# Performance work log

Measured on AMD Instinct MI355X. Metric: run time of the kernel, lower is better.

## Reference

```python
import jax, jax.numpy as jnp
import numpy as np

N_NODES = 50000
N_EDGES = 800000
IN_DIM = 256
HID = 32
HEADS = 8
OUT_DIM = 16
NEG_SLOPE = 0.2


def setup_inputs() -> dict:
    key = jax.random.key(0)
    ks = jax.random.split(key, 12)
    s = 0.05
    return {
        "emb": jax.random.normal(ks[0], (N_NODES, IN_DIM), jnp.float32),
        "src": jax.random.randint(ks[1], (N_EDGES,), 0, N_NODES),
        "dst": jax.random.randint(ks[2], (N_EDGES,), 0, N_NODES),
        "W1": jax.random.normal(ks[3], (IN_DIM, HEADS * HID), jnp.float32) * s,
        "attn_l1": jax.random.normal(ks[4], (HEADS, HID), jnp.float32) * s,
        "attn_r1": jax.random.normal(ks[5], (HEADS, HID), jnp.float32) * s,
        "bias1": jax.random.normal(ks[6], (HEADS * HID,), jnp.float32) * s,
        "W2": jax.random.normal(ks[7], (HEADS * HID, OUT_DIM), jnp.float32) * s,
        "attn_l2": jax.random.normal(ks[8], (1, OUT_DIM), jnp.float32) * s,
        "attn_r2": jax.random.normal(ks[9], (1, OUT_DIM), jnp.float32) * s,
        "bias2": jax.random.normal(ks[10], (OUT_DIM,), jnp.float32) * s,
    }


def gat_conv(x, src, dst, W, attn_l, attn_r, bias, n_heads, d_out):
    # x: [N, F_in] -> per-head projection h: [N, H, D]
    n = x.shape[0]
    h = (x @ W).reshape(n, n_heads, d_out)
    el = jnp.sum(h * attn_l, axis=-1)  # [N, H]
    er = jnp.sum(h * attn_r, axis=-1)  # [N, H]
    # edge scores with LeakyReLU (DGL negative_slope=0.2)
    e = jax.nn.leaky_relu(el[src] + er[dst], NEG_SLOPE)  # [E, H]
    # edge softmax over incoming edges of each destination node
    m = jax.ops.segment_max(e, dst, num_segments=n)  # [N, H]
    ee = jnp.exp(e - m[dst])
    denom = jax.ops.segment_sum(ee, dst, num_segments=n)  # [N, H]
    alpha = ee / denom[dst]  # [E, H]
    # weighted scatter-sum aggregation
    out = jax.ops.segment_sum(h[src] * alpha[:, :, None], dst, num_segments=n)  # [N, H, D]
    return out + bias.reshape(1, n_heads, d_out)


def reference(emb, src, dst, W1, attn_l1, attn_r1, bias1, W2, attn_l2, attn_r2, bias2):
    h = gat_conv(emb, src, dst, W1, attn_l1, attn_r1, bias1, HEADS, HID)  # [N, 8, 32]
    h = jax.nn.elu(h.reshape(N_NODES, HEADS * HID))  # [N, 256]
    out = gat_conv(h, src, dst, W2, attn_l2, attn_r2, bias2, 1, OUT_DIM)  # [N, 1, 16]
    return jnp.squeeze(out, axis=1)  # [N, 16]
```

## Files before the change

### kernel.cpp

```cpp
#include <hip/hip_runtime.h>
#include <math.h>

#define N_NODES 50000
#define N_EDGES 800000
#define NEG_SLOPE 0.2f

typedef __attribute__((ext_vector_type(8))) short bf16x8;
typedef __attribute__((ext_vector_type(4))) float f32x4;
typedef __attribute__((ext_vector_type(4))) _Float16 half4;

__device__ inline unsigned short f32_to_bf16_rn(float x) {
    unsigned u = __builtin_bit_cast(unsigned, x);
    unsigned r = u + 0x7fffu + ((u >> 16) & 1u);
    return (unsigned short)(r >> 16);
}
__device__ inline float bf16_bits_to_f32(unsigned short h) {
    unsigned u = ((unsigned)h) << 16;
    return __builtin_bit_cast(float, u);
}
__device__ inline void load_lds16(const void* g, void* l) {
    __builtin_amdgcn_global_load_lds(
        (const __attribute__((address_space(1))) void*)g,
        (__attribute__((address_space(3))) void*)l, 16, 0, 0);
}


__global__ void count_deg(const int* __restrict__ dst, int* __restrict__ deg) {
    int i = blockIdx.x * 256 + threadIdx.x;
    if (i < N_EDGES) atomicAdd(&deg[dst[i]], 1);
}

__global__ void scan_block(const int* __restrict__ deg, int* __restrict__ tmp,
                           int* __restrict__ bsum) {
    __shared__ int buf[256];
    int tid = threadIdx.x;
    int i = blockIdx.x * 256 + tid;
    int v = (i < N_NODES) ? deg[i] : 0;
    buf[tid] = v;
    __syncthreads();
    for (int off = 1; off < 256; off <<= 1) {
        int x = (tid >= off) ? buf[tid - off] : 0;
        __syncthreads();
        buf[tid] += x;
        __syncthreads();
    }
    if (i < N_NODES) tmp[i] = buf[tid];
    if (tid == 255) bsum[blockIdx.x] = buf[255];
}

__global__ void scan_bsum(int* __restrict__ bsum, int nb) {
    __shared__ int buf[256];
    int tid = threadIdx.x;
    int v = (tid < nb) ? bsum[tid] : 0;
    buf[tid] = v;
    __syncthreads();
    for (int off = 1; off < 256; off <<= 1) {
        int x = (tid >= off) ? buf[tid - off] : 0;
        __syncthreads();
        buf[tid] += x;
        __syncthreads();
    }
    if (tid < nb) bsum[tid] = buf[tid] - v;
}

__global__ void finalize_offs(const int* __restrict__ tmp, const int* __restrict__ deg,
                              const int* __restrict__ bsum, int* __restrict__ offs,
                              int* __restrict__ cursor) {
    int i = blockIdx.x * 256 + threadIdx.x;
    if (i < N_NODES) {
        int incl = tmp[i] + bsum[i >> 8];
        offs[i + 1] = incl;
        cursor[i] = incl - deg[i];
        if (i == 0) offs[0] = 0;
    }
}

__global__ void scatter_edges(const int* __restrict__ src, const int* __restrict__ dst,
                              int* __restrict__ cursor, int* __restrict__ src_csr) {
    int i = blockIdx.x * 256 + threadIdx.x;
    if (i < N_EDGES) {
        int p = atomicAdd(&cursor[dst[i]], 1);
        src_csr[p] = src[i];
    }
}


__global__ void convert_W1T(const float* __restrict__ W,
                            unsigned short* __restrict__ Th,
                            unsigned short* __restrict__ Tl) {
    int n = blockIdx.x;
    int k = threadIdx.x;
    float x = W[k * 256 + n];
    unsigned short h = f32_to_bf16_rn(x);
    float lo = x - bf16_bits_to_f32(h);
    size_t idx = ((size_t)(k >> 3) * 256 + n) * 8 + (k & 7);
    Th[idx] = h;
    Tl[idx] = f32_to_bf16_rn(lo);
}


__global__ __launch_bounds__(256) void gemm1_fused(const float* __restrict__ A,
                                                   const unsigned short* __restrict__ BTh,
                                                   const unsigned short* __restrict__ BTl,
                                                   const float* __restrict__ al,
                                                   const float* __restrict__ ar,
                                                   _Float16* __restrict__ C,
                                                   float* __restrict__ el,
                                                   float* __restrict__ er, int M) {
    __shared__ unsigned short Ah[4][64][8], Al[4][64][8];
    __shared__ unsigned short Bh[4][256][8], Bl[4][256][8];
    int tid = threadIdx.x;
    int lane = tid & 63, wave = tid >> 6;
    int kgl = lane >> 4, rl = lane & 15;
    int row0 = blockIdx.x * 64;

    f32x4 acc[4][4];
#pragma unroll
    for (int i = 0; i < 4; i++)
#pragma unroll
        for (int j = 0; j < 4; j++) acc[i][j] = (f32x4){0.f, 0.f, 0.f, 0.f};

    for (int k0 = 0; k0 < 256; k0 += 32) {
        int s0 = k0 >> 3;
#pragma unroll
        for (int i = 0; i < 4; i++) {
            load_lds16(&BTh[((size_t)(s0 + i) * 256 + tid) * 8], &Bh[i][wave << 6][0]);
            load_lds16(&BTl[((size_t)(s0 + i) * 256 + tid) * 8], &Bl[i][wave << 6][0]);
        }
        {
            int row = tid >> 2, kg = tid & 3;
            int gr = row0 + row;
            float4 x0 = make_float4(0.f, 0.f, 0.f, 0.f);
            float4 x1 = make_float4(0.f, 0.f, 0.f, 0.f);
            if (gr < M) {
                const float* p = &A[(size_t)gr * 256 + k0 + kg * 8];
                x0 = *reinterpret_cast<const float4*>(p);
                x1 = *reinterpret_cast<const float4*>(p + 4);
            }
            float xs[8] = {x0.x, x0.y, x0.z, x0.w, x1.x, x1.y, x1.z, x1.w};
            unsigned short hs[8], ls[8];
#pragma unroll
            for (int j = 0; j < 8; j++) {
                hs[j] = f32_to_bf16_rn(xs[j]);
                ls[j] = f32_to_bf16_rn(xs[j] - bf16_bits_to_f32(hs[j]));
            }
            *reinterpret_cast<bf16x8*>(&Ah[kg][row][0]) = *reinterpret_cast<bf16x8*>(hs);
            *reinterpret_cast<bf16x8*>(&Al[kg][row][0]) = *reinterpret_cast<bf16x8*>(ls);
        }
        __syncthreads();
        bf16x8 a_h[4], a_l[4];
#pragma unroll
        for (int mf = 0; mf < 4; mf++) {
            int row = mf * 16 + rl;
            a_h[mf] = *reinterpret_cast<bf16x8*>(&Ah[kgl][row][0]);
            a_l[mf] = *reinterpret_cast<bf16x8*>(&Al[kgl][row][0]);
        }
#pragma unroll
        for (int nf = 0; nf < 4; nf++) {
            int col = wave * 64 + nf * 16 + rl;
            bf16x8 bh = *reinterpret_cast<bf16x8*>(&Bh[kgl][col][0]);
            bf16x8 bl = *reinterpret_cast<bf16x8*>(&Bl[kgl][col][0]);
#pragma unroll
            for (int mf = 0; mf < 4; mf++) {
                acc[mf][nf] = __builtin_amdgcn_mfma_f32_16x16x32_bf16(a_h[mf], bh, acc[mf][nf], 0, 0, 0);
                acc[mf][nf] = __builtin_amdgcn_mfma_f32_16x16x32_bf16(a_h[mf], bl, acc[mf][nf], 0, 0, 0);
                acc[mf][nf] = __builtin_amdgcn_mfma_f32_16x16x32_bf16(a_l[mf], bh, acc[mf][nf], 0, 0, 0);
            }
        }
        __syncthreads();
    }
    float alv[4], arv[4];
#pragma unroll
    for (int nf = 0; nf < 4; nf++) {
        int c = wave * 64 + nf * 16 + rl;
        alv[nf] = al[c];
        arv[nf] = ar[c];
    }
#pragma unroll
    for (int mf = 0; mf < 4; mf++) {
#pragma unroll
        for (int rr = 0; rr < 4; rr++) {
            int grow = row0 + mf * 16 + (lane >> 4) * 4 + rr;
            bool ok = grow < M;
            if (ok) {
#pragma unroll
                for (int nf = 0; nf < 4; nf++) {
                    int gcol = wave * 64 + nf * 16 + rl;
                    C[(size_t)grow * 256 + gcol] = (_Float16)acc[mf][nf][rr];
                }
            }
            float e0 = acc[mf][0][rr] * alv[0] + acc[mf][1][rr] * alv[1];
            float e1 = acc[mf][2][rr] * alv[2] + acc[mf][3][rr] * alv[3];
            float f0 = acc[mf][0][rr] * arv[0] + acc[mf][1][rr] * arv[1];
            float f1 = acc[mf][2][rr] * arv[2] + acc[mf][3][rr] * arv[3];
#pragma unroll
            for (int off = 8; off >= 1; off >>= 1) {
                e0 += __shfl_down(e0, off, 16);
                e1 += __shfl_down(e1, off, 16);
                f0 += __shfl_down(f0, off, 16);
                f1 += __shfl_down(f1, off, 16);
            }
            if (rl == 0 && ok) {
                int h0 = wave * 2;
                el[grow * 8 + h0] = e0;
                el[grow * 8 + h0 + 1] = e1;
                er[grow * 8 + h0] = f0;
                er[grow * 8 + h0 + 1] = f1;
            }
        }
    }
}


__global__ __launch_bounds__(64) void agg1_fused(const int* __restrict__ offs,
                                                 const int* __restrict__ src_csr,
                                                 const float* __restrict__ el,
                                                 const float* __restrict__ er,
                                                 const _Float16* __restrict__ h1h,
                                                 const float* __restrict__ bias1,
                                                 _Float16* __restrict__ x2) {
    __shared__ float sc[64][8];
    int v = blockIdx.x;
    int t = threadIdx.x;
    int head = t >> 3, slot = t & 7;
    int start = offs[v], end = offs[v + 1];
    int deg = end - start;
    int ncache = (deg < 64) ? deg : 64;
    float erv = er[v * 8 + head];
    float s = 0.f;
    for (int base = 0; base < ncache; base += 8) {
        int e = base + slot;
        if (e < ncache) {
            int u = src_csr[start + e];
            float x = el[u * 8 + head] + erv;
            x = (x >= 0.f) ? x : NEG_SLOPE * x;
            float ex = expf(x);
            sc[e][head] = ex;
            s += ex;
        }
    }
    for (int base = 64; base < deg; base += 8) {
        int e = base + slot;
        if (e < deg) {
            int u = src_csr[start + e];
            float x = el[u * 8 + head] + erv;
            x = (x >= 0.f) ? x : NEG_SLOPE * x;
            s += expf(x);
        }
    }
    s += __shfl_xor(s, 1);
    s += __shfl_xor(s, 2);
    s += __shfl_xor(s, 4);
    float invs = (s > 0.f) ? 1.f / s : 0.f;
    __syncthreads();
    float4 acc = make_float4(0.f, 0.f, 0.f, 0.f);
    int i = start;
    for (; i + 3 < end && (i - start) + 3 < 64; i += 4) {
        int e = i - start;
        int u0 = src_csr[i];
        int u1 = src_csr[i + 1];
        int u2 = src_csr[i + 2];
        int u3 = src_csr[i + 3];
        float a0 = sc[e][head] * invs;
        float a1 = sc[e + 1][head] * invs;
        float a2 = sc[e + 2][head] * invs;
        float a3 = sc[e + 3][head] * invs;
        half4 p0 = *reinterpret_cast<const half4*>(&h1h[(size_t)u0 * 256 + 4 * t]);
        half4 p1 = *reinterpret_cast<const half4*>(&h1h[(size_t)u1 * 256 + 4 * t]);
        half4 p2 = *reinterpret_cast<const half4*>(&h1h[(size_t)u2 * 256 + 4 * t]);
        half4 p3 = *reinterpret_cast<const half4*>(&h1h[(size_t)u3 * 256 + 4 * t]);
        acc.x += a0 * (float)p0[0] + a1 * (float)p1[0] + a2 * (float)p2[0] + a3 * (float)p3[0];
        acc.y += a0 * (float)p0[1] + a1 * (float)p1[1] + a2 * (float)p2[1] + a3 * (float)p3[1];
        acc.z += a0 * (float)p0[2] + a1 * (float)p1[2] + a2 * (float)p2[2] + a3 * (float)p3[2];
        acc.w += a0 * (float)p0[3] + a1 * (float)p1[3] + a2 * (float)p2[3] + a3 * (float)p3[3];
    }
    for (; i < end; i++) {
        int e = i - start;
        int u0 = src_csr[i];
        float a0;
        if (e < 64) {
            a0 = sc[e][head] * invs;
        } else {
            float x = el[u0 * 8 + head] + erv;
            x = (x >= 0.f) ? x : NEG_SLOPE * x;
            a0 = expf(x) * invs;
        }
        half4 p0 = *reinterpret_cast<const half4*>(&h1h[(size_t)u0 * 256 + 4 * t]);
        acc.x += a0 * (float)p0[0];
        acc.y += a0 * (float)p0[1];
        acc.z += a0 * (float)p0[2];
        acc.w += a0 * (float)p0[3];
    }
    float4 b = *reinterpret_cast<const float4*>(&bias1[4 * t]);
    float ox = acc.x + b.x, oy = acc.y + b.y, oz = acc.z + b.z, ow = acc.w + b.w;
    ox = (ox > 0.f) ? ox : (expf(ox) - 1.f);
    oy = (oy > 0.f) ? oy : (expf(oy) - 1.f);
    oz = (oz > 0.f) ? oz : (expf(oz) - 1.f);
    ow = (ow > 0.f) ? ow : (expf(ow) - 1.f);
    half4 o = {(_Float16)ox, (_Float16)oy, (_Float16)oz, (_Float16)ow};
    *reinterpret_cast<half4*>(&x2[(size_t)v * 256 + 4 * t]) = o;
}


__global__ __launch_bounds__(256) void gemm2_mfma(const _Float16* __restrict__ X,
                                                  const float* __restrict__ W2,
                                                  const float* __restrict__ al,
                                                  const float* __restrict__ ar,
                                                  float* __restrict__ h2,
                                                  float* __restrict__ el2,
                                                  float* __restrict__ er2, int M) {
    __shared__ unsigned short Xh[4][64][8], Xl[4][64][8];
    __shared__ unsigned short Wh[32][16][8], Wl[32][16][8];
    int tid = threadIdx.x;
    int lane = tid & 63, wave = tid >> 6;
    int kgl = lane >> 4, rl = lane & 15;
    int row0 = blockIdx.x * 64;

#pragma unroll
    for (int j = 0; j < 16; j++) {
        int e = tid * 16 + j;
        float x = W2[e];
        unsigned short h = f32_to_bf16_rn(x);
        unsigned short l = f32_to_bf16_rn(x - bf16_bits_to_f32(h));
        int k = e >> 4, c = e & 15;
        Wh[k >> 3][c][k & 7] = h;
        Wl[k >> 3][c][k & 7] = l;
    }
    __syncthreads();

    f32x4 acc = (f32x4){0.f, 0.f, 0.f, 0.f};
    for (int k0 = 0; k0 < 256; k0 += 32) {
        {
            int row = tid >> 2, kg = tid & 3;
            int gr = row0 + row;
            unsigned short hs[8], ls[8];
            if (gr < M) {
                half4 x0 = *reinterpret_cast<const half4*>(&X[(size_t)gr * 256 + k0 + kg * 8]);
                half4 x1 = *reinterpret_cast<const half4*>(&X[(size_t)gr * 256 + k0 + kg * 8 + 4]);
                float xs[8] = {(float)x0[0], (float)x0[1], (float)x0[2], (float)x0[3],
                               (float)x1[0], (float)x1[1], (float)x1[2], (float)x1[3]};
#pragma unroll
                for (int j = 0; j < 8; j++) {
                    hs[j] = f32_to_bf16_rn(xs[j]);
                    ls[j] = f32_to_bf16_rn(xs[j] - bf16_bits_to_f32(hs[j]));
                }
            } else {
#pragma unroll
                for (int j = 0; j < 8; j++) { hs[j] = 0; ls[j] = 0; }
            }
            *reinterpret_cast<bf16x8*>(&Xh[kg][row][0]) = *reinterpret_cast<bf16x8*>(hs);
            *reinterpret_cast<bf16x8*>(&Xl[kg][row][0]) = *reinterpret_cast<bf16x8*>(ls);
        }
        __syncthreads();
        bf16x8 a_h = *reinterpret_cast<bf16x8*>(&Xh[kgl][wave * 16 + rl][0]);
        bf16x8 a_l = *reinterpret_cast<bf16x8*>(&Xl[kgl][wave * 16 + rl][0]);
        int kg = (k0 >> 3) + kgl;
        bf16x8 b_h = *reinterpret_cast<bf16x8*>(&Wh[kg][rl][0]);
        bf16x8 b_l = *reinterpret_cast<bf16x8*>(&Wl[kg][rl][0]);
        acc = __builtin_amdgcn_mfma_f32_16x16x32_bf16(a_h, b_h, acc, 0, 0, 0);
        acc = __builtin_amdgcn_mfma_f32_16x16x32_bf16(a_h, b_l, acc, 0, 0, 0);
        acc = __builtin_amdgcn_mfma_f32_16x16x32_bf16(a_l, b_h, acc, 0, 0, 0);
        __syncthreads();
    }
    float alv = al[rl], arv = ar[rl];
#pragma unroll
    for (int rr = 0; rr < 4; rr++) {
        int grow = row0 + wave * 16 + (lane >> 4) * 4 + rr;
        bool ok = grow < M;
        if (ok) h2[(size_t)grow * 16 + rl] = acc[rr];
        float pl = acc[rr] * alv;
        float pr = acc[rr] * arv;
#pragma unroll
        for (int off = 8; off >= 1; off >>= 1) {
            pl += __shfl_down(pl, off, 16);
            pr += __shfl_down(pr, off, 16);
        }
        if (rl == 0 && ok) {
            el2[grow] = pl;
            er2[grow] = pr;
        }
    }
}


__global__ __launch_bounds__(64) void agg2_fused(const int* __restrict__ offs,
                                                 const int* __restrict__ src_csr,
                                                 const float* __restrict__ el2,
                                                 const float* __restrict__ er2,
                                                 const float* __restrict__ h2,
                                                 const float* __restrict__ bias2,
                                                 float* __restrict__ out) {
    int v = blockIdx.x;
    int t = threadIdx.x;
    int start = offs[v], end = offs[v + 1];
    float erv = er2[v];
    float s = 0.f;
    for (int i = start + t; i < end; i += 64) {
        int u = src_csr[i];
        float x = el2[u] + erv;
        x = (x >= 0.f) ? x : NEG_SLOPE * x;
        s += expf(x);
    }
#pragma unroll
    for (int off = 32; off >= 1; off >>= 1) s += __shfl_xor(s, off);
    float invs = (s > 0.f) ? 1.f / s : 0.f;
    int eg = t >> 4, d = t & 15;
    float acc = 0.f;
    for (int i = start + eg; i < end; i += 4) {
        int u = src_csr[i];
        float x = el2[u] + erv;
        x = (x >= 0.f) ? x : NEG_SLOPE * x;
        acc += expf(x) * invs * h2[(size_t)u * 16 + d];
    }
    acc += __shfl_xor(acc, 32);
    acc += __shfl_xor(acc, 16);
    if (t < 16) out[(size_t)v * 16 + t] = acc + bias2[t];
}


extern "C" void kernel_launch(void* const* d_in, const int* in_sizes, int n_in,
                              void* d_out, int out_size, void* d_ws, size_t ws_size,
                              hipStream_t stream) {
    const float* emb   = (const float*)d_in[0];
    const int*   src   = (const int*)d_in[1];
    const int*   dst   = (const int*)d_in[2];
    const float* W1    = (const float*)d_in[3];
    const float* al1   = (const float*)d_in[4];
    const float* ar1   = (const float*)d_in[5];
    const float* bias1 = (const float*)d_in[6];
    const float* W2    = (const float*)d_in[7];
    const float* al2   = (const float*)d_in[8];
    const float* ar2   = (const float*)d_in[9];
    const float* bias2 = (const float*)d_in[10];
    float* out = (float*)d_out;

    char* ws = (char*)d_ws;
    auto alloc = [&](size_t bytes) -> void* {
        void* p = ws;
        ws += (bytes + 255) & ~(size_t)255;
        return p;
    };
    int* deg     = (int*)alloc(N_NODES * 4);
    int* cursor  = (int*)alloc(N_NODES * 4);
    int* offs    = (int*)alloc((N_NODES + 1) * 4);
    int* tmp     = (int*)alloc(N_NODES * 4);
    int* bsum    = (int*)alloc(256 * 4);
    int* src_csr = (int*)alloc(N_EDGES * 4);
    unsigned short* W1Th = (unsigned short*)alloc(256 * 256 * 2);
    unsigned short* W1Tl = (unsigned short*)alloc(256 * 256 * 2);
    _Float16* h1h = (_Float16*)alloc((size_t)N_NODES * 256 * 2);
    float* el1   = (float*)alloc(N_NODES * 8 * 4);
    float* er1   = (float*)alloc(N_NODES * 8 * 4);
    _Float16* x2h = (_Float16*)alloc((size_t)N_NODES * 256 * 2);
    float* h2    = (float*)alloc((size_t)N_NODES * 16 * 4);
    float* el2   = (float*)alloc(N_NODES * 4);
    float* er2   = (float*)alloc(N_NODES * 4);

    int nb = (N_NODES + 255) / 256;

    hipMemsetAsync(deg, 0, N_NODES * 4, stream);
    count_deg<<<(N_EDGES + 255) / 256, 256, 0, stream>>>(dst, deg);
    scan_block<<<nb, 256, 0, stream>>>(deg, tmp, bsum);
    scan_bsum<<<1, 256, 0, stream>>>(bsum, nb);
    finalize_offs<<<nb, 256, 0, stream>>>(tmp, deg, bsum, offs, cursor);
    scatter_edges<<<(N_EDGES + 255) / 256, 256, 0, stream>>>(src, dst, cursor, src_csr);

    convert_W1T<<<256, 256, 0, stream>>>(W1, W1Th, W1Tl);
    gemm1_fused<<<(N_NODES + 63) / 64, 256, 0, stream>>>(emb, W1Th, W1Tl, al1, ar1,
                                                         h1h, el1, er1, N_NODES);
    agg1_fused<<<N_NODES, 64, 0, stream>>>(offs, src_csr, el1, er1, h1h, bias1, x2h);
    gemm2_mfma<<<(N_NODES + 63) / 64, 256, 0, stream>>>(x2h, W2, al2, ar2, h2, el2, er2, N_NODES);
    agg2_fused<<<N_NODES, 64, 0, stream>>>(offs, src_csr, el2, er2, h2, bias2, out);
}
```

Measured before the change: 254.4 us.

## Fuse block-sum scan into finalize, prefetch GEMM1 A, widen GEMM2 K-steps, cache agg2 scores

Drops the separate scan_bsum launch by having each finalize block reduce the preceding block sums itself. GEMM1 now register-prefetches the next A tile while the current step computes, to hide global-load latency. GEMM2 stages 128 K-values per barrier instead of 32, cutting synchronisations from eight rounds to two at the cost of more LDS. agg2 caches up to 64 per-edge exp scores in shared memory so the second pass skips recomputing them.

```diff
diff --git a/kernel.cpp b/kernel.cpp
--- a/kernel.cpp
+++ b/kernel.cpp
@@ -48,27 +48,22 @@
     if (tid == 255) bsum[blockIdx.x] = buf[255];
 }
 
-__global__ void scan_bsum(int* __restrict__ bsum, int nb) {
-    __shared__ int buf[256];
-    int tid = threadIdx.x;
-    int v = (tid < nb) ? bsum[tid] : 0;
-    buf[tid] = v;
-    __syncthreads();
-    for (int off = 1; off < 256; off <<= 1) {
-        int x = (tid >= off) ? buf[tid - off] : 0;
-        __syncthreads();
-        buf[tid] += x;
-        __syncthreads();
-    }
-    if (tid < nb) bsum[tid] = buf[tid] - v;
-}
-
 __global__ void finalize_offs(const int* __restrict__ tmp, const int* __restrict__ deg,
                               const int* __restrict__ bsum, int* __restrict__ offs,
-                              int* __restrict__ cursor) {
-    int i = blockIdx.x * 256 + threadIdx.x;
+                              int* __restrict__ cursor, int nb) {
+    __shared__ int red[256];
+    int tid = threadIdx.x;
+    int b = blockIdx.x;
+    red[tid] = (tid < nb && tid < b) ? bsum[tid] : 0;
+    __syncthreads();
+    for (int off = 128; off > 0; off >>= 1) {
+        if (tid < off) red[tid] += red[tid + off];
+        __syncthreads();
+    }
+    int prefix = red[0];
+    int i = b * 256 + tid;
     if (i < N_NODES) {
-        int incl = tmp[i] + bsum[i >> 8];
+        int incl = tmp[i] + prefix;
         offs[i + 1] = incl;
         cursor[i] = incl - deg[i];
         if (i == 0) offs[0] = 0;
@@ -120,34 +115,40 @@
 #pragma unroll
         for (int j = 0; j < 4; j++) acc[i][j] = (f32x4){0.f, 0.f, 0.f, 0.f};
 
-    for (int k0 = 0; k0 < 256; k0 += 32) {
+    int rowA = tid >> 2, kgA = tid & 3;
+    int grA = row0 + rowA;
+    const float* pA = &A[(size_t)grA * 256 + kgA * 8];
+    float4 x0 = make_float4(0.f, 0.f, 0.f, 0.f);
+    float4 x1 = make_float4(0.f, 0.f, 0.f, 0.f);
+    if (grA < M) {
+        x0 = *reinterpret_cast<const float4*>(pA);
+        x1 = *reinterpret_cast<const float4*>(pA + 4);
+    }
+
+    for (int step = 0; step < 8; step++) {
+        int k0 = step * 32;
+        {
+            float xs[8] = {x0.x, x0.y, x0.z, x0.w, x1.x, x1.y, x1.z, x1.w};
+            unsigned short hs[8], ls[8];
+#pragma unroll
+            for (int j = 0; j < 8; j++) {
+                hs[j] = f32_to_bf16_rn(xs[j]);
+                ls[j] = f32_to_bf16_rn(xs[j] - bf16_bits_to_f32(hs[j]));
+            }
+            *reinterpret_cast<bf16x8*>(&Ah[kgA][rowA][0]) = *reinterpret_cast<bf16x8*>(hs);
+            *reinterpret_cast<bf16x8*>(&Al[kgA][rowA][0]) = *reinterpret_cast<bf16x8*>(ls);
+        }
         int s0 = k0 >> 3;
 #pragma unroll
         for (int i = 0; i < 4; i++) {
             load_lds16(&BTh[((size_t)(s0 + i) * 256 + tid) * 8], &Bh[i][wave << 6][0]);
             load_lds16(&BTl[((size_t)(s0 + i) * 256 + tid) * 8], &Bl[i][wave << 6][0]);
         }
-        {
-            int row = tid >> 2, kg = tid & 3;
-            int gr = row0 + row;
-            float4 x0 = make_float4(0.f, 0.f, 0.f, 0.f);
-            float4 x1 = make_float4(0.f, 0.f, 0.f, 0.f);
-            if (gr < M) {
-                const float* p = &A[(size_t)gr * 256 + k0 + kg * 8];
-                x0 = *reinterpret_cast<const float4*>(p);
-                x1 = *reinterpret_cast<const float4*>(p + 4);
-            }
-            float xs[8] = {x0.x, x0.y, x0.z, x0.w, x1.x, x1.y, x1.z, x1.w};
-            unsigned short hs[8], ls[8];
-#pragma unroll
-            for (int j = 0; j < 8; j++) {
-                hs[j] = f32_to_bf16_rn(xs[j]);
-                ls[j] = f32_to_bf16_rn(xs[j] - bf16_bits_to_f32(hs[j]));
-            }
-            *reinterpret_cast<bf16x8*>(&Ah[kg][row][0]) = *reinterpret_cast<bf16x8*>(hs);
-            *reinterpret_cast<bf16x8*>(&Al[kg][row][0]) = *reinterpret_cast<bf16x8*>(ls);
-        }
-        __syncthreads();
+        __syncthreads();
+        if (step < 7 && grA < M) {
+            x0 = *reinterpret_cast<const float4*>(pA + (step + 1) * 32);
+            x1 = *reinterpret_cast<const float4*>(pA + (step + 1) * 32 + 4);
+        }
         bf16x8 a_h[4], a_l[4];
 #pragma unroll
         for (int mf = 0; mf < 4; mf++) {
@@ -309,7 +310,7 @@
                                                   float* __restrict__ h2,
                                                   float* __restrict__ el2,
                                                   float* __restrict__ er2, int M) {
-    __shared__ unsigned short Xh[4][64][8], Xl[4][64][8];
+    __shared__ unsigned short Xh[16][64][8], Xl[16][64][8];
     __shared__ unsigned short Wh[32][16][8], Wl[32][16][8];
     int tid = threadIdx.x;
     int lane = tid & 63, wave = tid >> 6;
@@ -326,40 +327,46 @@
         Wh[k >> 3][c][k & 7] = h;
         Wl[k >> 3][c][k & 7] = l;
     }
-    __syncthreads();
 
     f32x4 acc = (f32x4){0.f, 0.f, 0.f, 0.f};
-    for (int k0 = 0; k0 < 256; k0 += 32) {
-        {
-            int row = tid >> 2, kg = tid & 3;
-            int gr = row0 + row;
+    int rowX = tid >> 2, kgb = (tid & 3) * 4;
+    int grX = row0 + rowX;
+    for (int step = 0; step < 2; step++) {
+#pragma unroll
+        for (int j = 0; j < 4; j++) {
+            int kg = kgb + j;
+            int kglob = step * 128 + kg * 8;
             unsigned short hs[8], ls[8];
-            if (gr < M) {
-                half4 x0 = *reinterpret_cast<const half4*>(&X[(size_t)gr * 256 + k0 + kg * 8]);
-                half4 x1 = *reinterpret_cast<const half4*>(&X[(size_t)gr * 256 + k0 + kg * 8 + 4]);
-                float xs[8] = {(float)x0[0], (float)x0[1], (float)x0[2], (float)x0[3],
-                               (float)x1[0], (float)x1[1], (float)x1[2], (float)x1[3]};
-#pragma unroll
-                for (int j = 0; j < 8; j++) {
-                    hs[j] = f32_to_bf16_rn(xs[j]);
-                    ls[j] = f32_to_bf16_rn(xs[j] - bf16_bits_to_f32(hs[j]));
+            if (grX < M) {
+                half4 a0 = *reinterpret_cast<const half4*>(&X[(size_t)grX * 256 + kglob]);
+                half4 a1 = *reinterpret_cast<const half4*>(&X[(size_t)grX * 256 + kglob + 4]);
+                float xs[8] = {(float)a0[0], (float)a0[1], (float)a0[2], (float)a0[3],
+                               (float)a1[0], (float)a1[1], (float)a1[2], (float)a1[3]};
+#pragma unroll
+                for (int q = 0; q < 8; q++) {
+                    hs[q] = f32_to_bf16_rn(xs[q]);
+                    ls[q] = f32_to_bf16_rn(xs[q] - bf16_bits_to_f32(hs[q]));
                 }
             } else {
 #pragma unroll
-                for (int j = 0; j < 8; j++) { hs[j] = 0; ls[j] = 0; }
-            }
-            *reinterpret_cast<bf16x8*>(&Xh[kg][row][0]) = *reinterpret_cast<bf16x8*>(hs);
-            *reinterpret_cast<bf16x8*>(&Xl[kg][row][0]) = *reinterpret_cast<bf16x8*>(ls);
-        }
-        __syncthreads();
-        bf16x8 a_h = *reinterpret_cast<bf16x8*>(&Xh[kgl][wave * 16 + rl][0]);
-        bf16x8 a_l = *reinterpret_cast<bf16x8*>(&Xl[kgl][wave * 16 + rl][0]);
-        int kg = (k0 >> 3) + kgl;
-        bf16x8 b_h = *reinterpret_cast<bf16x8*>(&Wh[kg][rl][0]);
-        bf16x8 b_l = *reinterpret_cast<bf16x8*>(&Wl[kg][rl][0]);
-        acc = __builtin_amdgcn_mfma_f32_16x16x32_bf16(a_h, b_h, acc, 0, 0, 0);
-        acc = __builtin_amdgcn_mfma_f32_16x16x32_bf16(a_h, b_l, acc, 0, 0, 0);
-        acc = __builtin_amdgcn_mfma_f32_16x16x32_bf16(a_l, b_h, acc, 0, 0, 0);
+                for (int q = 0; q < 8; q++) { hs[q] = 0; ls[q] = 0; }
+            }
+            *reinterpret_cast<bf16x8*>(&Xh[kg][rowX][0]) = *reinterpret_cast<bf16x8*>(hs);
+            *reinterpret_cast<bf16x8*>(&Xl[kg][rowX][0]) = *reinterpret_cast<bf16x8*>(ls);
+        }
+        __syncthreads();
+#pragma unroll
+        for (int ks = 0; ks < 4; ks++) {
+            int kg = ks * 4 + kgl;
+            int kgw = step * 16 + kg;
+            bf16x8 a_h = *reinterpret_cast<bf16x8*>(&Xh[kg][wave * 16 + rl][0]);
+            bf16x8 a_l = *reinterpret_cast<bf16x8*>(&Xl[kg][wave * 16 + rl][0]);
+            bf16x8 b_h = *reinterpret_cast<bf16x8*>(&Wh[kgw][rl][0]);
+            bf16x8 b_l = *reinterpret_cast<bf16x8*>(&Wl[kgw][rl][0]);
+            acc = __builtin_amdgcn_mfma_f32_16x16x32_bf16(a_h, b_h, acc, 0, 0, 0);
+            acc = __builtin_amdgcn_mfma_f32_16x16x32_bf16(a_h, b_l, acc, 0, 0, 0);
+            acc = __builtin_amdgcn_mfma_f32_16x16x32_bf16(a_l, b_h, acc, 0, 0, 0);
+        }
         __syncthreads();
     }
     float alv = al[rl], arv = ar[rl];
@@ -390,13 +397,24 @@
                                                  const float* __restrict__ h2,
                                                  const float* __restrict__ bias2,
                                                  float* __restrict__ out) {
+    __shared__ float sc2[64];
     int v = blockIdx.x;
     int t = threadIdx.x;
     int start = offs[v], end = offs[v + 1];
+    int deg = end - start;
+    int ncache = (deg < 64) ? deg : 64;
     float erv = er2[v];
     float s = 0.f;
-    for (int i = start + t; i < end; i += 64) {
-        int u = src_csr[i];
+    for (int e = t; e < ncache; e += 64) {
+        int u = src_csr[start + e];
+        float x = el2[u] + erv;
+        x = (x >= 0.f) ? x : NEG_SLOPE * x;
+        float ex = expf(x);
+        sc2[e] = ex;
+        s += ex;
+    }
+    for (int e = 64 + t; e < deg; e += 64) {
+        int u = src_csr[start + e];
         float x = el2[u] + erv;
         x = (x >= 0.f) ? x : NEG_SLOPE * x;
         s += expf(x);
@@ -404,13 +422,21 @@
 #pragma unroll
     for (int off = 32; off >= 1; off >>= 1) s += __shfl_xor(s, off);
     float invs = (s > 0.f) ? 1.f / s : 0.f;
+    __syncthreads();
     int eg = t >> 4, d = t & 15;
     float acc = 0.f;
     for (int i = start + eg; i < end; i += 4) {
+        int e = i - start;
         int u = src_csr[i];
-        float x = el2[u] + erv;
-        x = (x >= 0.f) ? x : NEG_SLOPE * x;
-        acc += expf(x) * invs * h2[(size_t)u * 16 + d];
+        float a;
+        if (e < 64) {
+            a = sc2[e] * invs;
+        } else {
+            float x = el2[u] + erv;
+            x = (x >= 0.f) ? x : NEG_SLOPE * x;
+            a = expf(x) * invs;
+        }
+        acc += a * h2[(size_t)u * 16 + d];
     }
     acc += __shfl_xor(acc, 32);
     acc += __shfl_xor(acc, 16);
@@ -461,8 +487,7 @@
     hipMemsetAsync(deg, 0, N_NODES * 4, stream);
     count_deg<<<(N_EDGES + 255) / 256, 256, 0, stream>>>(dst, deg);
     scan_block<<<nb, 256, 0, stream>>>(deg, tmp, bsum);
-    scan_bsum<<<1, 256, 0, stream>>>(bsum, nb);
-    finalize_offs<<<nb, 256, 0, stream>>>(tmp, deg, bsum, offs, cursor);
+    finalize_offs<<<nb, 256, 0, stream>>>(tmp, deg, bsum, offs, cursor, nb);
     scatter_edges<<<(N_EDGES + 255) / 256, 256, 0, stream>>>(src, dst, cursor, src_csr);
 
     convert_W1T<<<256, 256, 0, stream>>>(W1, W1Th, W1Tl);
```

After: 255.2 us. Within noise of the previous version (+0.3%).
